# Kernel optimization log

Hardware: AMD Instinct MI355X
Metric: run time of the kernel (lower is better)

## Reference

```python
import jax, jax.numpy as jnp
import numpy as np

N, E, F, R, S = 20000, 320000, 64, 8, 10
AVG_NEIGH = 16.0


def setup_inputs() -> dict:
    key = jax.random.key(0)
    ks = jax.random.split(key, 16)
    inp = {
        "vectors": jax.random.normal(ks[0], (E, 3), jnp.float32),
        "node_feats": jax.random.normal(ks[1], (N, F, 4), jnp.float32),  # [N, F, 1(0e)+3(1o)]
        "node_specie": jax.random.randint(ks[2], (N,), 0, S),
        "radial_embedding": jax.random.normal(ks[3], (E, R), jnp.float32),
        "senders": jax.random.randint(ks[4], (E,), 0, N),
        "receivers": jax.random.randint(ks[5], (E,), 0, N),
        # residual FullyConnectedTensorProduct(feats, one-hot species 0e) == species-dep. linear per l
        "W_res_s": jax.random.normal(ks[6], (S, F, F), jnp.float32),
        "W_res_v": jax.random.normal(ks[7], (S, F, F), jnp.float32),
        # interaction block: input linear per l
        "W_in_s": jax.random.normal(ks[8], (F, F), jnp.float32),
        "W_in_v": jax.random.normal(ks[9], (F, F), jnp.float32),
        # radial MLP -> 5 CG tensor-product path weights per channel
        "mlp_w1": jax.random.normal(ks[10], (R, 64), jnp.float32),
        "mlp_w2": jax.random.normal(ks[11], (64, 5 * F), jnp.float32) / 8.0,
        # interaction block: output linear per l
        "W_out_s": jax.random.normal(ks[12], (F, F), jnp.float32),
        "W_out_v": jax.random.normal(ks[13], (F, F), jnp.float32),
        # symmetric product basis (correlation 3), species-dependent term weights
        "W_prod_s": jax.random.normal(ks[14], (S, 5, F), jnp.float32) * 0.3,
        "W_prod_v": jax.random.normal(ks[15], (S, 4, F), jnp.float32) * 0.3,
    }
    k2 = jax.random.split(jax.random.key(1), 3)
    inp["W_lin_s"] = jax.random.normal(k2[0], (F, F), jnp.float32)
    inp["W_lin_v"] = jax.random.normal(k2[1], (F, F), jnp.float32)
    inp["W_read"] = jax.random.normal(k2[2], (F, 1), jnp.float32)
    return inp


def _forward(vectors, node_feats, node_specie, radial_embedding, senders, receivers,
             W_res_s, W_res_v, W_in_s, W_in_v, mlp_w1, mlp_w2, W_out_s, W_out_v,
             W_prod_s, W_prod_v, W_lin_s, W_lin_v, W_read):
    inv_sf = 1.0 / jnp.sqrt(jnp.float32(F))
    s = node_feats[..., 0]          # [N,F]   0e channels
    v = node_feats[..., 1:]         # [N,F,3] 1o channels

    # --- residual connection: FCTP(feats, one-hot species 0e attrs) -> species-gated linear per l
    res_s = jnp.einsum('nf,ngf->ng', s, W_res_s[node_specie]) * inv_sf
    res_v = jnp.einsum('nfc,ngf->ngc', v, W_res_v[node_specie]) * inv_sf

    # --- InteractionBlock ---
    h_s = (s @ W_in_s) * inv_sf
    h_v = jnp.einsum('nfc,fg->ngc', v, W_in_v) * inv_sf

    # spherical harmonics up to max_ell=1: Y0 = 1, Y1 = unit edge vector
    r = jnp.sqrt(jnp.sum(vectors * vectors, -1) + 1e-12)
    Y1 = vectors / r[:, None]                                # [E,3]

    # radial MLP produces per-edge weights for the 5 CG paths:
    # (0e x Y0 -> 0e), (1o . Y1 -> 0e), (0e x Y1 -> 1o), (1o x Y0 -> 1o), (1o x Y1 -> 1o, cross)
    w = (jax.nn.silu(radial_embedding @ mlp_w1) @ mlp_w2).reshape(-1, 5, F)  # [E,5,F]

    ss = h_s[senders]                                        # [E,F]
    sv = h_v[senders]                                        # [E,F,3]
    dot = jnp.einsum('efc,ec->ef', sv, Y1)                   # [E,F]
    m_s = w[:, 0] * ss + w[:, 1] * dot                       # [E,F]
    m_v = (w[:, 2] * ss)[:, :, None] * Y1[:, None, :] \
        + w[:, 3][:, :, None] * sv \
        + w[:, 4][:, :, None] * jnp.cross(sv, Y1[:, None, :])  # [E,F,3]

    agg_s = jnp.zeros_like(h_s).at[receivers].add(m_s) / AVG_NEIGH
    agg_v = jnp.zeros_like(h_v).at[receivers].add(m_v) / AVG_NEIGH
    a_s = (agg_s @ W_out_s) * inv_sf
    a_v = jnp.einsum('nfc,fg->ngc', agg_v, W_out_v) * inv_sf

    # --- EquivariantProductBasisBlock: correlation-3 symmetric contraction, species-dependent ---
    vv = jnp.sum(a_v * a_v, -1)                              # [N,F] invariant |v|^2
    Wp = W_prod_s[node_specie]                               # [N,5,F]
    p_s = (Wp[:, 0] * a_s + Wp[:, 1] * a_s ** 2 + Wp[:, 2] * a_s ** 3
           + Wp[:, 3] * vv + Wp[:, 4] * a_s * vv)
    Wv = W_prod_v[node_specie]                               # [N,4,F]
    p_v = (Wv[:, 0] + Wv[:, 1] * a_s + Wv[:, 2] * a_s ** 2 + Wv[:, 3] * vv)[:, :, None] * a_v

    f_s = (p_s @ W_lin_s) * inv_sf + res_s
    f_v = jnp.einsum('nfc,fg->ngc', p_v, W_lin_v) * inv_sf + res_v

    # --- LinearReadoutBlock (output_irreps = 0e), 1 head ---
    node_out = ((f_s @ W_read) * inv_sf)[:, None, :]         # [N, heads=1, 1]
    new_feats = jnp.concatenate([f_s[..., None], f_v], axis=-1)  # [N,F,4]
    return node_out, new_feats


def reference(vectors, node_feats, node_specie, radial_embedding, senders, receivers,
              W_res_s, W_res_v, W_in_s, W_in_v, mlp_w1, mlp_w2, W_out_s, W_out_v,
              W_prod_s, W_prod_v, W_lin_s, W_lin_v, W_read):
    return _forward(vectors, node_feats, node_specie, radial_embedding, senders, receivers,
                    W_res_s, W_res_v, W_in_s, W_in_v, mlp_w1, mlp_w2, W_out_s, W_out_v,
                    W_prod_s, W_prod_v, W_lin_s, W_lin_v, W_read)
```

## Files before the change

### kernel.cpp

```cpp
#include <hip/hip_runtime.h>
#include <math.h>

#define NN 20000
#define NE 320000
#define NF (NN*64)
#define TB 16

typedef float v2f __attribute__((ext_vector_type(2)));

#if __has_builtin(__builtin_elementwise_fma)
#define PKFMA(a,b,c) __builtin_elementwise_fma(a,b,c)
#else
static __device__ __forceinline__ v2f PKFMA(v2f a, v2f b, v2f c){
  v2f r; r.x = fmaf(a.x,b.x,c.x); r.y = fmaf(a.y,b.y,c.y); return r;
}
#endif

__global__ __launch_bounds__(256) void k_pre(
    const float* __restrict__ node_feats, const float* __restrict__ W_in_s,
    const float* __restrict__ W_in_v, float* __restrict__ h,
    const int* __restrict__ receivers, int* __restrict__ count, int* __restrict__ rank,
    const float* __restrict__ Ws, const float* __restrict__ Wv,
    float* __restrict__ Wst, float* __restrict__ Wvt)
{
  __shared__ float sh[16][4][64];
  if(blockIdx.x >= 1250){
    int b = blockIdx.x - 1250;
    int e = b*256 + threadIdx.x;
    rank[e] = atomicAdd(&count[receivers[e]], 1);
    if(b < 160){
      int i = b*256 + threadIdx.x;
      int spec = i >> 12;
      int g = (i >> 6) & 63;
      int f = i & 63;
      Wst[spec*4096 + f*64 + g] = Ws[i];
      Wvt[spec*4096 + f*64 + g] = Wv[i];
    }
    return;
  }
  int wave = threadIdx.x >> 6, lane = threadIdx.x & 63;
  int nb = blockIdx.x*16 + wave*4;
  #pragma unroll
  for(int k=0;k<4;++k){
    int nd = wave*4 + k;
    float4 nf = *(const float4*)(node_feats + (size_t)((nb+k)*64 + lane)*4);
    sh[nd][0][lane]=nf.x; sh[nd][1][lane]=nf.y; sh[nd][2][lane]=nf.z; sh[nd][3][lane]=nf.w;
  }
  __syncthreads();
  float as[4]={0,0,0,0}, a0[4]={0,0,0,0}, a1[4]={0,0,0,0}, a2[4]={0,0,0,0};
  for(int f=0; f<64; ++f){
    float ws = W_in_s[f*64+lane], wv = W_in_v[f*64+lane];
    #pragma unroll
    for(int k=0;k<4;++k){
      int nd = wave*4 + k;
      as[k] = fmaf(sh[nd][0][f], ws, as[k]);
      a0[k] = fmaf(sh[nd][1][f], wv, a0[k]);
      a1[k] = fmaf(sh[nd][2][f], wv, a1[k]);
      a2[k] = fmaf(sh[nd][3][f], wv, a2[k]);
    }
  }
  #pragma unroll
  for(int k=0;k<4;++k){
    float4 o4; o4.x = as[k]*0.125f; o4.y = a0[k]*0.125f;
    o4.z = a1[k]*0.125f; o4.w = a2[k]*0.125f;
    *(float4*)(h + (size_t)((nb+k)*64 + lane)*4) = o4;
  }
}

__global__ __launch_bounds__(1024) void k_scan(const int* __restrict__ count,
                                               int* __restrict__ offset)
{
  __shared__ int part[1024];
  int t = threadIdx.x;
  const int PER = 20;
  int base = t*PER;
  int loc[PER];
  int s = 0;
  #pragma unroll
  for(int i=0;i<PER;++i){
    int idx = base+i;
    int v = (idx < NN) ? count[idx] : 0;
    loc[i] = v; s += v;
  }
  part[t] = s;
  __syncthreads();
  for(int off=1; off<1024; off<<=1){
    int v = (t>=off) ? part[t-off] : 0;
    __syncthreads();
    part[t] += v;
    __syncthreads();
  }
  int run = t ? part[t-1] : 0;
  #pragma unroll
  for(int i=0;i<PER;++i){
    int idx = base+i;
    if(idx < NN) offset[idx] = run;
    run += loc[i];
  }
  if(t==1023) offset[NN] = part[1023];
}

__global__ __launch_bounds__(256) void k_scatter(
    const int* __restrict__ senders, const int* __restrict__ receivers,
    const float* __restrict__ vectors, const float* __restrict__ radial,
    const int* __restrict__ offset, const int* __restrict__ rank,
    float* __restrict__ rec)
{
  int e = blockIdx.x*256 + threadIdx.x;
  int r = receivers[e];
  int slot = offset[r] + rank[e];
  float vx = vectors[e*3], vy = vectors[e*3+1], vz = vectors[e*3+2];
  float rinv = rsqrtf(vx*vx + vy*vy + vz*vz + 1e-12f);
  float4 ra = *(const float4*)(radial + (size_t)e*8);
  float4 rb = *(const float4*)(radial + (size_t)e*8 + 4);
  float* rp = rec + (size_t)slot*16;
  float4 w0; w0.x = vx*rinv; w0.y = vy*rinv; w0.z = vz*rinv; w0.w = __int_as_float(senders[e]);
  float4 w3; w3.x = __int_as_float(r); w3.y = 0.f; w3.z = 0.f; w3.w = 0.f;
  *(float4*)(rp)      = w0;
  *(float4*)(rp + 4)  = ra;
  *(float4*)(rp + 8)  = rb;
  *(float4*)(rp + 12) = w3;
}

__global__ __launch_bounds__(256) void k_edge(
    const float* __restrict__ rec,
    const float* __restrict__ mlp_w1, const float* __restrict__ mlp_w2,
    const float* __restrict__ h, float* __restrict__ agg)
{
  __shared__ float recS[4][256];
  __shared__ float hid[4][64][18];
  int tid = threadIdx.x;
  int wave = tid >> 6, lane = tid & 63;
  int e0 = (blockIdx.x*4 + wave)*TB;

  *(float4*)&recS[wave][lane*4] = *(const float4*)(rec + (size_t)e0*16 + lane*4);

  float wl[8];
  #pragma unroll
  for(int r=0;r<8;++r) wl[r] = mlp_w1[r*64+lane];

  #pragma unroll
  for(int t=0;t<TB;++t){
    float acc = 0.f;
    #pragma unroll
    for(int r=0;r<8;++r) acc = fmaf(recS[wave][t*16+4+r], wl[r], acc);
    hid[wave][lane][t] = acc / (1.f + __expf(-acc));
  }

  float as_=0.f, av0=0.f, av1=0.f, av2=0.f;
  int cur = __float_as_int(recS[wave][12]);

  #pragma unroll 1
  for(int half=0; half<2; ++half){
    int tb = half*8;

    float4 hv4[8];
    #pragma unroll
    for(int p=0;p<8;++p){
      int snd = __float_as_int(recS[wave][(tb+p)*16+3]);
      hv4[p] = *(const float4*)(h + (size_t)(snd*64 + lane)*4);
    }

    v2f wv[5][4];
    #pragma unroll
    for(int j=0;j<5;++j)
      #pragma unroll
      for(int tp=0;tp<4;++tp) wv[j][tp] = (v2f){0.f, 0.f};

    for(int hh=0; hh<64; hh+=2){
      float b0[5], b1[5];
      #pragma unroll
      for(int j=0;j<5;++j){
        b0[j] = mlp_w2[hh*320     + j*64 + lane];
        b1[j] = mlp_w2[(hh+1)*320 + j*64 + lane];
      }
      #pragma unroll
      for(int tp=0;tp<4;++tp){
        v2f h0 = *(const v2f*)&hid[wave][hh][tb + 2*tp];
        v2f h1 = *(const v2f*)&hid[wave][hh+1][tb + 2*tp];
        #pragma unroll
        for(int j=0;j<5;++j){
          v2f bb0 = {b0[j], b0[j]};
          v2f bb1 = {b1[j], b1[j]};
          wv[j][tp] = PKFMA(bb0, h0, wv[j][tp]);
          wv[j][tp] = PKFMA(bb1, h1, wv[j][tp]);
        }
      }
    }

    #pragma unroll
    for(int i=0;i<8;++i){
      int t = tb + i;
      float4 hc = hv4[i];
      int rcv = __float_as_int(recS[wave][t*16+12]);
      if(rcv != cur){
        size_t ro = (size_t)cur*256 + lane;
        atomicAdd(&agg[ro],     as_);
        atomicAdd(&agg[ro+64],  av0);
        atomicAdd(&agg[ro+128], av1);
        atomicAdd(&agg[ro+192], av2);
        as_=0.f; av0=0.f; av1=0.f; av2=0.f;
        cur = rcv;
      }
      float y0=recS[wave][t*16], y1=recS[wave][t*16+1], y2=recS[wave][t*16+2];
      float ss=hc.x, sv0=hc.y, sv1=hc.z, sv2=hc.w;
      float dot = sv0*y0 + sv1*y1 + sv2*y2;
      float wt0 = wv[0][i>>1][i&1], wt1 = wv[1][i>>1][i&1];
      float wt2 = wv[2][i>>1][i&1], wt3 = wv[3][i>>1][i&1], wt4 = wv[4][i>>1][i&1];
      as_ += wt0*ss + wt1*dot;
      float w2s = wt2*ss;
      av0 += w2s*y0 + wt3*sv0 + wt4*(sv1*y2 - sv2*y1);
      av1 += w2s*y1 + wt3*sv1 + wt4*(sv2*y0 - sv0*y2);
      av2 += w2s*y2 + wt3*sv2 + wt4*(sv0*y1 - sv1*y0);
    }
  }
  size_t ro = (size_t)cur*256 + lane;
  atomicAdd(&agg[ro],     as_);
  atomicAdd(&agg[ro+64],  av0);
  atomicAdd(&agg[ro+128], av1);
  atomicAdd(&agg[ro+192], av2);
}

__global__ __launch_bounds__(256) void k_node_post(
  const float* __restrict__ node_feats, const int* __restrict__ specie,
  const float* __restrict__ agg,
  const float* __restrict__ Wrst, const float* __restrict__ Wrvt,
  const float* __restrict__ W_out_s, const float* __restrict__ W_out_v,
  const float* __restrict__ W_prod_s, const float* __restrict__ W_prod_v,
  const float* __restrict__ W_lin_s, const float* __restrict__ W_lin_v,
  const float* __restrict__ W_read, float* __restrict__ out_node,
  float* __restrict__ out_feats)
{
  __shared__ float shA[16][4][64];
  __shared__ float shS[16][4][64];
  int wave = threadIdx.x >> 6, lane = threadIdx.x & 63;
  int nb = blockIdx.x*16 + wave*4;
  #pragma unroll
  for(int k=0;k<4;++k){
    int nd = wave*4 + k;
    size_t o = (size_t)(nb+k)*256 + lane;
    shA[nd][0][lane] = agg[o]      * (1.f/16.f);
    shA[nd][1][lane] = agg[o+64]   * (1.f/16.f);
    shA[nd][2][lane] = agg[o+128]  * (1.f/16.f);
    shA[nd][3][lane] = agg[o+192]  * (1.f/16.f);
    float4 nf = *(const float4*)(node_feats + (size_t)((nb+k)*64 + lane)*4);
    shS[nd][0][lane]=nf.x; shS[nd][1][lane]=nf.y; shS[nd][2][lane]=nf.z; shS[nd][3][lane]=nf.w;
  }
  int spec[4];
  #pragma unroll
  for(int k=0;k<4;++k) spec[k] = specie[nb+k];
  __syncthreads();
  float a_s[4]={0,0,0,0}, a0[4]={0,0,0,0}, a1[4]={0,0,0,0}, a2[4]={0,0,0,0};
  float r_s[4]={0,0,0,0}, r0[4]={0,0,0,0}, r1[4]={0,0,0,0}, r2[4]={0,0,0,0};
  for(int f=0; f<64; ++f){
    float wos = W_out_s[f*64+lane], wov = W_out_v[f*64+lane];
    #pragma unroll
    for(int k=0;k<4;++k){
      int nd = wave*4 + k;
      a_s[k] = fmaf(shA[nd][0][f], wos, a_s[k]);
      a0[k]  = fmaf(shA[nd][1][f], wov, a0[k]);
      a1[k]  = fmaf(shA[nd][2][f], wov, a1[k]);
      a2[k]  = fmaf(shA[nd][3][f], wov, a2[k]);
    }
    #pragma unroll
    for(int k=0;k<4;++k){
      int nd = wave*4 + k;
      float wrs = Wrst[spec[k]*4096 + f*64 + lane];
      float wrv = Wrvt[spec[k]*4096 + f*64 + lane];
      r_s[k] = fmaf(shS[nd][0][f], wrs, r_s[k]);
      r0[k]  = fmaf(shS[nd][1][f], wrv, r0[k]);
      r1[k]  = fmaf(shS[nd][2][f], wrv, r1[k]);
      r2[k]  = fmaf(shS[nd][3][f], wrv, r2[k]);
    }
  }
  __syncthreads();
  #pragma unroll
  for(int k=0;k<4;++k){
    int nd = wave*4 + k;
    float A_s = a_s[k]*0.125f, A0 = a0[k]*0.125f, A1 = a1[k]*0.125f, A2 = a2[k]*0.125f;
    float vv = A0*A0 + A1*A1 + A2*A2;
    float as2 = A_s*A_s;
    const float* Wp = W_prod_s + spec[k]*320;
    float p_s = Wp[lane]*A_s + Wp[64+lane]*as2 + Wp[128+lane]*as2*A_s
              + Wp[192+lane]*vv + Wp[256+lane]*A_s*vv;
    const float* Wq = W_prod_v + spec[k]*256;
    float coef = Wq[lane] + Wq[64+lane]*A_s + Wq[128+lane]*as2 + Wq[192+lane]*vv;
    shS[nd][0][lane] = p_s;
    shS[nd][1][lane] = coef*A0;
    shS[nd][2][lane] = coef*A1;
    shS[nd][3][lane] = coef*A2;
  }
  __syncthreads();
  float lfs[4]={0,0,0,0}, lf0[4]={0,0,0,0}, lf1[4]={0,0,0,0}, lf2[4]={0,0,0,0};
  for(int f=0; f<64; ++f){
    float wls = W_lin_s[f*64+lane], wlv = W_lin_v[f*64+lane];
    #pragma unroll
    for(int k=0;k<4;++k){
      int nd = wave*4 + k;
      lfs[k] = fmaf(shS[nd][0][f], wls, lfs[k]);
      lf0[k] = fmaf(shS[nd][1][f], wlv, lf0[k]);
      lf1[k] = fmaf(shS[nd][2][f], wlv, lf1[k]);
      lf2[k] = fmaf(shS[nd][3][f], wlv, lf2[k]);
    }
  }
  float wr = W_read[lane];
  #pragma unroll
  for(int k=0;k<4;++k){
    int n = nb + k;
    float FS = lfs[k]*0.125f + r_s[k]*0.125f;
    float F0 = lf0[k]*0.125f + r0[k]*0.125f;
    float F1 = lf1[k]*0.125f + r1[k]*0.125f;
    float F2 = lf2[k]*0.125f + r2[k]*0.125f;
    float x = FS * wr;
    #pragma unroll
    for(int off=32; off; off>>=1) x += __shfl_down(x, off);
    if(lane==0) out_node[n] = x*0.125f;
    float4 o4; o4.x=FS; o4.y=F0; o4.z=F1; o4.w=F2;
    *(float4*)(out_feats + (size_t)(n*64+lane)*4) = o4;
  }
}

extern "C" void kernel_launch(void* const* d_in, const int* in_sizes, int n_in,
                              void* d_out, int out_size, void* d_ws, size_t ws_size,
                              hipStream_t stream) {
  const float* vectors    = (const float*)d_in[0];
  const float* node_feats = (const float*)d_in[1];
  const int*   node_specie= (const int*)  d_in[2];
  const float* radial     = (const float*)d_in[3];
  const int*   senders    = (const int*)  d_in[4];
  const int*   receivers  = (const int*)  d_in[5];
  const float* W_res_s    = (const float*)d_in[6];
  const float* W_res_v    = (const float*)d_in[7];
  const float* W_in_s     = (const float*)d_in[8];
  const float* W_in_v     = (const float*)d_in[9];
  const float* mlp_w1     = (const float*)d_in[10];
  const float* mlp_w2     = (const float*)d_in[11];
  const float* W_out_s    = (const float*)d_in[12];
  const float* W_out_v    = (const float*)d_in[13];
  const float* W_prod_s   = (const float*)d_in[14];
  const float* W_prod_v   = (const float*)d_in[15];
  const float* W_lin_s    = (const float*)d_in[16];
  const float* W_lin_v    = (const float*)d_in[17];
  const float* W_read     = (const float*)d_in[18];

  float* ws   = (float*)d_ws;
  float* h    = ws;
  float* agg  = ws + 4*(size_t)NF;
  float* Wrst = ws + 8*(size_t)NF;
  float* Wrvt = Wrst + 40960;
  float* rec  = Wrvt + 40960;
  int*   rank   = (int*)(rec + 16*(size_t)NE);
  int*   offset = rank + NE;
  int*   count  = offset + NN + 1;

  hipMemsetAsync(agg,   0, (size_t)4*NF*sizeof(float), stream);
  hipMemsetAsync(count, 0, (size_t)NN*sizeof(int), stream);
  k_pre<<<2500, 256, 0, stream>>>(node_feats, W_in_s, W_in_v, h,
                                  receivers, count, rank,
                                  W_res_s, W_res_v, Wrst, Wrvt);
  k_scan   <<<1,     1024, 0, stream>>>(count, offset);
  k_scatter<<<NE/256, 256, 0, stream>>>(senders, receivers, vectors, radial,
                                        offset, rank, rec);
  k_edge<<<NE/64, 256, 0, stream>>>(rec, mlp_w1, mlp_w2, h, agg);
  k_node_post<<<NN/16, 256, 0, stream>>>(node_feats, node_specie, agg,
                                         Wrst, Wrvt, W_out_s, W_out_v,
                                         W_prod_s, W_prod_v, W_lin_s, W_lin_v,
                                         W_read, (float*)d_out, (float*)d_out + NN);
}
```

Baseline: 465.1 us.

## Compute all 16 edge weights in one pass and double node tiles per block

The edge kernel now computes the radial MLP second layer for all 16 edges in a single loop over the hidden dimension instead of two halves. Each mlp_w2 load is reused across twice as many edges. The sender feature gathers are rotated as a four-deep prefetch ring inside the aggregation loop. The node pre and post kernels process 8 nodes per wave instead of 4, doubling weight reuse per load. The cost is much higher register pressure (80 accumulator floats in the edge kernel, 64 in node_post) and more LDS, which may lower occupancy.

Result: no change. 474.3 us (+2.0%).

```diff
diff --git a/kernel.cpp b/kernel.cpp
--- a/kernel.cpp
+++ b/kernel.cpp
@@ -23,9 +23,9 @@
     const float* __restrict__ Ws, const float* __restrict__ Wv,
     float* __restrict__ Wst, float* __restrict__ Wvt)
 {
-  __shared__ float sh[16][4][64];
-  if(blockIdx.x >= 1250){
-    int b = blockIdx.x - 1250;
+  __shared__ float sh[32][4][64];
+  if(blockIdx.x >= 625){
+    int b = blockIdx.x - 625;
     int e = b*256 + threadIdx.x;
     rank[e] = atomicAdd(&count[receivers[e]], 1);
     if(b < 160){
@@ -39,20 +39,21 @@
     return;
   }
   int wave = threadIdx.x >> 6, lane = threadIdx.x & 63;
-  int nb = blockIdx.x*16 + wave*4;
-  #pragma unroll
-  for(int k=0;k<4;++k){
-    int nd = wave*4 + k;
+  int nb = blockIdx.x*32 + wave*8;
+  #pragma unroll
+  for(int k=0;k<8;++k){
+    int nd = wave*8 + k;
     float4 nf = *(const float4*)(node_feats + (size_t)((nb+k)*64 + lane)*4);
     sh[nd][0][lane]=nf.x; sh[nd][1][lane]=nf.y; sh[nd][2][lane]=nf.z; sh[nd][3][lane]=nf.w;
   }
   __syncthreads();
-  float as[4]={0,0,0,0}, a0[4]={0,0,0,0}, a1[4]={0,0,0,0}, a2[4]={0,0,0,0};
+  float as[8]={0,0,0,0,0,0,0,0}, a0[8]={0,0,0,0,0,0,0,0};
+  float a1[8]={0,0,0,0,0,0,0,0}, a2[8]={0,0,0,0,0,0,0,0};
   for(int f=0; f<64; ++f){
     float ws = W_in_s[f*64+lane], wv = W_in_v[f*64+lane];
     #pragma unroll
-    for(int k=0;k<4;++k){
-      int nd = wave*4 + k;
+    for(int k=0;k<8;++k){
+      int nd = wave*8 + k;
       as[k] = fmaf(sh[nd][0][f], ws, as[k]);
       a0[k] = fmaf(sh[nd][1][f], wv, a0[k]);
       a1[k] = fmaf(sh[nd][2][f], wv, a1[k]);
@@ -60,7 +61,7 @@
     }
   }
   #pragma unroll
-  for(int k=0;k<4;++k){
+  for(int k=0;k<8;++k){
     float4 o4; o4.x = as[k]*0.125f; o4.y = a0[k]*0.125f;
     o4.z = a1[k]*0.125f; o4.w = a2[k]*0.125f;
     *(float4*)(h + (size_t)((nb+k)*64 + lane)*4) = o4;
@@ -128,7 +129,7 @@
     const float* __restrict__ h, float* __restrict__ agg)
 {
   __shared__ float recS[4][256];
-  __shared__ float hid[4][64][18];
+  __shared__ float hid[4][64][20];
   int tid = threadIdx.x;
   int wave = tid >> 6, lane = tid & 63;
   int e0 = (blockIdx.x*4 + wave)*TB;
@@ -147,72 +148,63 @@
     hid[wave][lane][t] = acc / (1.f + __expf(-acc));
   }
 
+  v2f wv[5][8];
+  #pragma unroll
+  for(int j=0;j<5;++j)
+    #pragma unroll
+    for(int tp=0;tp<8;++tp) wv[j][tp] = (v2f){0.f, 0.f};
+  const float* w2p = mlp_w2 + lane;
+  for(int hh=0; hh<64; ++hh){
+    float b[5];
+    #pragma unroll
+    for(int j=0;j<5;++j) b[j] = w2p[hh*320 + j*64];
+    v2f hv[8];
+    #pragma unroll
+    for(int tp=0;tp<8;++tp) hv[tp] = *(const v2f*)&hid[wave][hh][2*tp];
+    #pragma unroll
+    for(int j=0;j<5;++j){
+      v2f bb = {b[j], b[j]};
+      #pragma unroll
+      for(int tp=0;tp<8;++tp) wv[j][tp] = PKFMA(bb, hv[tp], wv[j][tp]);
+    }
+  }
+
+  float4 hv4[4];
+  #pragma unroll
+  for(int p=0;p<4;++p){
+    int snd = __float_as_int(recS[wave][p*16+3]);
+    hv4[p] = *(const float4*)(h + (size_t)(snd*64 + lane)*4);
+  }
+
   float as_=0.f, av0=0.f, av1=0.f, av2=0.f;
   int cur = __float_as_int(recS[wave][12]);
-
-  #pragma unroll 1
-  for(int half=0; half<2; ++half){
-    int tb = half*8;
-
-    float4 hv4[8];
-    #pragma unroll
-    for(int p=0;p<8;++p){
-      int snd = __float_as_int(recS[wave][(tb+p)*16+3]);
-      hv4[p] = *(const float4*)(h + (size_t)(snd*64 + lane)*4);
-    }
-
-    v2f wv[5][4];
-    #pragma unroll
-    for(int j=0;j<5;++j)
-      #pragma unroll
-      for(int tp=0;tp<4;++tp) wv[j][tp] = (v2f){0.f, 0.f};
-
-    for(int hh=0; hh<64; hh+=2){
-      float b0[5], b1[5];
-      #pragma unroll
-      for(int j=0;j<5;++j){
-        b0[j] = mlp_w2[hh*320     + j*64 + lane];
-        b1[j] = mlp_w2[(hh+1)*320 + j*64 + lane];
-      }
-      #pragma unroll
-      for(int tp=0;tp<4;++tp){
-        v2f h0 = *(const v2f*)&hid[wave][hh][tb + 2*tp];
-        v2f h1 = *(const v2f*)&hid[wave][hh+1][tb + 2*tp];
-        #pragma unroll
-        for(int j=0;j<5;++j){
-          v2f bb0 = {b0[j], b0[j]};
-          v2f bb1 = {b1[j], b1[j]};
-          wv[j][tp] = PKFMA(bb0, h0, wv[j][tp]);
-          wv[j][tp] = PKFMA(bb1, h1, wv[j][tp]);
-        }
-      }
-    }
-
-    #pragma unroll
-    for(int i=0;i<8;++i){
-      int t = tb + i;
-      float4 hc = hv4[i];
-      int rcv = __float_as_int(recS[wave][t*16+12]);
-      if(rcv != cur){
-        size_t ro = (size_t)cur*256 + lane;
-        atomicAdd(&agg[ro],     as_);
-        atomicAdd(&agg[ro+64],  av0);
-        atomicAdd(&agg[ro+128], av1);
-        atomicAdd(&agg[ro+192], av2);
-        as_=0.f; av0=0.f; av1=0.f; av2=0.f;
-        cur = rcv;
-      }
-      float y0=recS[wave][t*16], y1=recS[wave][t*16+1], y2=recS[wave][t*16+2];
-      float ss=hc.x, sv0=hc.y, sv1=hc.z, sv2=hc.w;
-      float dot = sv0*y0 + sv1*y1 + sv2*y2;
-      float wt0 = wv[0][i>>1][i&1], wt1 = wv[1][i>>1][i&1];
-      float wt2 = wv[2][i>>1][i&1], wt3 = wv[3][i>>1][i&1], wt4 = wv[4][i>>1][i&1];
-      as_ += wt0*ss + wt1*dot;
-      float w2s = wt2*ss;
-      av0 += w2s*y0 + wt3*sv0 + wt4*(sv1*y2 - sv2*y1);
-      av1 += w2s*y1 + wt3*sv1 + wt4*(sv2*y0 - sv0*y2);
-      av2 += w2s*y2 + wt3*sv2 + wt4*(sv0*y1 - sv1*y0);
-    }
+  #pragma unroll
+  for(int t=0;t<TB;++t){
+    float4 hc = hv4[t&3];
+    if(t+4 < TB){
+      int snd = __float_as_int(recS[wave][(t+4)*16+3]);
+      hv4[t&3] = *(const float4*)(h + (size_t)(snd*64 + lane)*4);
+    }
+    int rcv = __float_as_int(recS[wave][t*16+12]);
+    if(rcv != cur){
+      size_t ro = (size_t)cur*256 + lane;
+      atomicAdd(&agg[ro],     as_);
+      atomicAdd(&agg[ro+64],  av0);
+      atomicAdd(&agg[ro+128], av1);
+      atomicAdd(&agg[ro+192], av2);
+      as_=0.f; av0=0.f; av1=0.f; av2=0.f;
+      cur = rcv;
+    }
+    float y0=recS[wave][t*16], y1=recS[wave][t*16+1], y2=recS[wave][t*16+2];
+    float ss=hc.x, sv0=hc.y, sv1=hc.z, sv2=hc.w;
+    float dot = sv0*y0 + sv1*y1 + sv2*y2;
+    float wt0 = wv[0][t>>1][t&1], wt1 = wv[1][t>>1][t&1];
+    float wt2 = wv[2][t>>1][t&1], wt3 = wv[3][t>>1][t&1], wt4 = wv[4][t>>1][t&1];
+    as_ += wt0*ss + wt1*dot;
+    float w2s = wt2*ss;
+    av0 += w2s*y0 + wt3*sv0 + wt4*(sv1*y2 - sv2*y1);
+    av1 += w2s*y1 + wt3*sv1 + wt4*(sv2*y0 - sv0*y2);
+    av2 += w2s*y2 + wt3*sv2 + wt4*(sv0*y1 - sv1*y0);
   }
   size_t ro = (size_t)cur*256 + lane;
   atomicAdd(&agg[ro],     as_);
@@ -231,13 +223,13 @@
   const float* __restrict__ W_read, float* __restrict__ out_node,
   float* __restrict__ out_feats)
 {
-  __shared__ float shA[16][4][64];
-  __shared__ float shS[16][4][64];
+  __shared__ float shA[32][4][64];
+  __shared__ float shS[32][4][64];
   int wave = threadIdx.x >> 6, lane = threadIdx.x & 63;
-  int nb = blockIdx.x*16 + wave*4;
-  #pragma unroll
-  for(int k=0;k<4;++k){
-    int nd = wave*4 + k;
+  int nb = blockIdx.x*32 + wave*8;
+  #pragma unroll
+  for(int k=0;k<8;++k){
+    int nd = wave*8 + k;
     size_t o = (size_t)(nb+k)*256 + lane;
     shA[nd][0][lane] = agg[o]      * (1.f/16.f);
     shA[nd][1][lane] = agg[o+64]   * (1.f/16.f);
@@ -246,25 +238,27 @@
     float4 nf = *(const float4*)(node_feats + (size_t)((nb+k)*64 + lane)*4);
     shS[nd][0][lane]=nf.x; shS[nd][1][lane]=nf.y; shS[nd][2][lane]=nf.z; shS[nd][3][lane]=nf.w;
   }
-  int spec[4];
-  #pragma unroll
-  for(int k=0;k<4;++k) spec[k] = specie[nb+k];
-  __syncthreads();
-  float a_s[4]={0,0,0,0}, a0[4]={0,0,0,0}, a1[4]={0,0,0,0}, a2[4]={0,0,0,0};
-  float r_s[4]={0,0,0,0}, r0[4]={0,0,0,0}, r1[4]={0,0,0,0}, r2[4]={0,0,0,0};
+  int spec[8];
+  #pragma unroll
+  for(int k=0;k<8;++k) spec[k] = specie[nb+k];
+  __syncthreads();
+  float a_s[8]={0,0,0,0,0,0,0,0}, a0[8]={0,0,0,0,0,0,0,0};
+  float a1[8]={0,0,0,0,0,0,0,0}, a2[8]={0,0,0,0,0,0,0,0};
+  float r_s[8]={0,0,0,0,0,0,0,0}, r0[8]={0,0,0,0,0,0,0,0};
+  float r1[8]={0,0,0,0,0,0,0,0}, r2[8]={0,0,0,0,0,0,0,0};
   for(int f=0; f<64; ++f){
     float wos = W_out_s[f*64+lane], wov = W_out_v[f*64+lane];
     #pragma unroll
-    for(int k=0;k<4;++k){
-      int nd = wave*4 + k;
+    for(int k=0;k<8;++k){
+      int nd = wave*8 + k;
       a_s[k] = fmaf(shA[nd][0][f], wos, a_s[k]);
       a0[k]  = fmaf(shA[nd][1][f], wov, a0[k]);
       a1[k]  = fmaf(shA[nd][2][f], wov, a1[k]);
       a2[k]  = fmaf(shA[nd][3][f], wov, a2[k]);
     }
     #pragma unroll
-    for(int k=0;k<4;++k){
-      int nd = wave*4 + k;
+    for(int k=0;k<8;++k){
+      int nd = wave*8 + k;
       float wrs = Wrst[spec[k]*4096 + f*64 + lane];
       float wrv = Wrvt[spec[k]*4096 + f*64 + lane];
       r_s[k] = fmaf(shS[nd][0][f], wrs, r_s[k]);
@@ -275,8 +269,8 @@
   }
   __syncthreads();
   #pragma unroll
-  for(int k=0;k<4;++k){
-    int nd = wave*4 + k;
+  for(int k=0;k<8;++k){
+    int nd = wave*8 + k;
     float A_s = a_s[k]*0.125f, A0 = a0[k]*0.125f, A1 = a1[k]*0.125f, A2 = a2[k]*0.125f;
     float vv = A0*A0 + A1*A1 + A2*A2;
     float as2 = A_s*A_s;
@@ -291,12 +285,13 @@
     shS[nd][3][lane] = coef*A2;
   }
   __syncthreads();
-  float lfs[4]={0,0,0,0}, lf0[4]={0,0,0,0}, lf1[4]={0,0,0,0}, lf2[4]={0,0,0,0};
+  float lfs[8]={0,0,0,0,0,0,0,0}, lf0[8]={0,0,0,0,0,0,0,0};
+  float lf1[8]={0,0,0,0,0,0,0,0}, lf2[8]={0,0,0,0,0,0,0,0};
   for(int f=0; f<64; ++f){
     float wls = W_lin_s[f*64+lane], wlv = W_lin_v[f*64+lane];
     #pragma unroll
-    for(int k=0;k<4;++k){
-      int nd = wave*4 + k;
+    for(int k=0;k<8;++k){
+      int nd = wave*8 + k;
       lfs[k] = fmaf(shS[nd][0][f], wls, lfs[k]);
       lf0[k] = fmaf(shS[nd][1][f], wlv, lf0[k]);
       lf1[k] = fmaf(shS[nd][2][f], wlv, lf1[k]);
@@ -305,7 +300,7 @@
   }
   float wr = W_read[lane];
   #pragma unroll
-  for(int k=0;k<4;++k){
+  for(int k=0;k<8;++k){
     int n = nb + k;
     float FS = lfs[k]*0.125f + r_s[k]*0.125f;
     float F0 = lf0[k]*0.125f + r0[k]*0.125f;
@@ -355,15 +350,15 @@
 
   hipMemsetAsync(agg,   0, (size_t)4*NF*sizeof(float), stream);
   hipMemsetAsync(count, 0, (size_t)NN*sizeof(int), stream);
-  k_pre<<<2500, 256, 0, stream>>>(node_feats, W_in_s, W_in_v, h,
+  k_pre<<<1875, 256, 0, stream>>>(node_feats, W_in_s, W_in_v, h,
                                   receivers, count, rank,
                                   W_res_s, W_res_v, Wrst, Wrvt);
   k_scan   <<<1,     1024, 0, stream>>>(count, offset);
   k_scatter<<<NE/256, 256, 0, stream>>>(senders, receivers, vectors, radial,
                                         offset, rank, rec);
   k_edge<<<NE/64, 256, 0, stream>>>(rec, mlp_w1, mlp_w2, h, agg);
-  k_node_post<<<NN/16, 256, 0, stream>>>(node_feats, node_specie, agg,
-                                         Wrst, Wrvt, W_out_s, W_out_v,
-                                         W_prod_s, W_prod_v, W_lin_s, W_lin_v,
-                                         W_read, (float*)d_out, (float*)d_out + NN);
-}
+  k_node_post<<<625, 256, 0, stream>>>(node_feats, node_specie, agg,
+                                       Wrst, Wrvt, W_out_s, W_out_v,
+                                       W_prod_s, W_prod_v, W_lin_s, W_lin_v,
+                                       W_read, (float*)d_out, (float*)d_out + NN);
+}
```

## Compute all 16 edge weights in one pass with relaid-out MLP weights

Applied to the files above, without the earlier changes.

The second radial MLP layer now runs over all 16 edges of a wave in a single pass instead of two halves. Each hh step loads its five weights with one vector load from a per-lane padded copy of mlp_w2 that k_pre builds, so mlp_w2 is read once rather than twice. Sender feature gathers use a four-deep rolling prefetch instead of eight loads per half. The single pass doubles the accumulator registers to 80 floats, which may lower occupancy, and the hid row is padded to 20 floats so the float4 reads from shared memory stay aligned.

After: 472.1 us. About the same (+1.5%).

```diff
diff --git a/kernel.cpp b/kernel.cpp
--- a/kernel.cpp
+++ b/kernel.cpp
@@ -21,7 +21,8 @@
     const float* __restrict__ W_in_v, float* __restrict__ h,
     const int* __restrict__ receivers, int* __restrict__ count, int* __restrict__ rank,
     const float* __restrict__ Ws, const float* __restrict__ Wv,
-    float* __restrict__ Wst, float* __restrict__ Wvt)
+    float* __restrict__ Wst, float* __restrict__ Wvt,
+    const float* __restrict__ w2, float* __restrict__ w2r)
 {
   __shared__ float sh[16][4][64];
   if(blockIdx.x >= 1250){
@@ -35,6 +36,13 @@
       int f = i & 63;
       Wst[spec*4096 + f*64 + g] = Ws[i];
       Wvt[spec*4096 + f*64 + g] = Wv[i];
+    } else if(b < 288){
+      int i = (b-160)*256 + threadIdx.x;
+      int hh = i >> 9;
+      int r  = i & 511;
+      int ln = r >> 3;
+      int j  = r & 7;
+      w2r[i] = (j < 5) ? w2[hh*320 + j*64 + ln] : 0.f;
     }
     return;
   }
@@ -124,11 +132,11 @@
 
 __global__ __launch_bounds__(256) void k_edge(
     const float* __restrict__ rec,
-    const float* __restrict__ mlp_w1, const float* __restrict__ mlp_w2,
+    const float* __restrict__ mlp_w1, const float* __restrict__ w2r,
     const float* __restrict__ h, float* __restrict__ agg)
 {
   __shared__ float recS[4][256];
-  __shared__ float hid[4][64][18];
+  __shared__ float hid[4][64][20];
   int tid = threadIdx.x;
   int wave = tid >> 6, lane = tid & 63;
   int e0 = (blockIdx.x*4 + wave)*TB;
@@ -147,72 +155,69 @@
     hid[wave][lane][t] = acc / (1.f + __expf(-acc));
   }
 
+  v2f wv[5][8];
+  #pragma unroll
+  for(int j=0;j<5;++j)
+    #pragma unroll
+    for(int tp=0;tp<8;++tp) wv[j][tp] = (v2f){0.f, 0.f};
+  const float* w2p = w2r + (size_t)lane*8;
+  for(int hh=0; hh<64; ++hh){
+    float4 b04 = *(const float4*)(w2p + hh*512);
+    float  b4  = w2p[hh*512 + 4];
+    float b[5] = {b04.x, b04.y, b04.z, b04.w, b4};
+    float4 q0 = *(const float4*)&hid[wave][hh][0];
+    float4 q1 = *(const float4*)&hid[wave][hh][4];
+    float4 q2 = *(const float4*)&hid[wave][hh][8];
+    float4 q3 = *(const float4*)&hid[wave][hh][12];
+    v2f hv[8];
+    hv[0] = (v2f){q0.x, q0.y}; hv[1] = (v2f){q0.z, q0.w};
+    hv[2] = (v2f){q1.x, q1.y}; hv[3] = (v2f){q1.z, q1.w};
+    hv[4] = (v2f){q2.x, q2.y}; hv[5] = (v2f){q2.z, q2.w};
+    hv[6] = (v2f){q3.x, q3.y}; hv[7] = (v2f){q3.z, q3.w};
+    #pragma unroll
+    for(int j=0;j<5;++j){
+      v2f bb = {b[j], b[j]};
+      #pragma unroll
+      for(int tp=0;tp<8;++tp) wv[j][tp] = PKFMA(bb, hv[tp], wv[j][tp]);
+    }
+  }
+
+  float4 hv4[4];
+  #pragma unroll
+  for(int p=0;p<4;++p){
+    int snd = __float_as_int(recS[wave][p*16+3]);
+    hv4[p] = *(const float4*)(h + (size_t)(snd*64 + lane)*4);
+  }
+
   float as_=0.f, av0=0.f, av1=0.f, av2=0.f;
   int cur = __float_as_int(recS[wave][12]);
-
-  #pragma unroll 1
-  for(int half=0; half<2; ++half){
-    int tb = half*8;
-
-    float4 hv4[8];
-    #pragma unroll
-    for(int p=0;p<8;++p){
-      int snd = __float_as_int(recS[wave][(tb+p)*16+3]);
-      hv4[p] = *(const float4*)(h + (size_t)(snd*64 + lane)*4);
-    }
-
-    v2f wv[5][4];
-    #pragma unroll
-    for(int j=0;j<5;++j)
-      #pragma unroll
-      for(int tp=0;tp<4;++tp) wv[j][tp] = (v2f){0.f, 0.f};
-
-    for(int hh=0; hh<64; hh+=2){
-      float b0[5], b1[5];
-      #pragma unroll
-      for(int j=0;j<5;++j){
-        b0[j] = mlp_w2[hh*320     + j*64 + lane];
-        b1[j] = mlp_w2[(hh+1)*320 + j*64 + lane];
-      }
-      #pragma unroll
-      for(int tp=0;tp<4;++tp){
-        v2f h0 = *(const v2f*)&hid[wave][hh][tb + 2*tp];
-        v2f h1 = *(const v2f*)&hid[wave][hh+1][tb + 2*tp];
-        #pragma unroll
-        for(int j=0;j<5;++j){
-          v2f bb0 = {b0[j], b0[j]};
-          v2f bb1 = {b1[j], b1[j]};
-          wv[j][tp] = PKFMA(bb0, h0, wv[j][tp]);
-          wv[j][tp] = PKFMA(bb1, h1, wv[j][tp]);
-        }
-      }
-    }
-
-    #pragma unroll
-    for(int i=0;i<8;++i){
-      int t = tb + i;
-      float4 hc = hv4[i];
-      int rcv = __float_as_int(recS[wave][t*16+12]);
-      if(rcv != cur){
-        size_t ro = (size_t)cur*256 + lane;
-        atomicAdd(&agg[ro],     as_);
-        atomicAdd(&agg[ro+64],  av0);
-        atomicAdd(&agg[ro+128], av1);
-        atomicAdd(&agg[ro+192], av2);
-        as_=0.f; av0=0.f; av1=0.f; av2=0.f;
-        cur = rcv;
-      }
-      float y0=recS[wave][t*16], y1=recS[wave][t*16+1], y2=recS[wave][t*16+2];
-      float ss=hc.x, sv0=hc.y, sv1=hc.z, sv2=hc.w;
-      float dot = sv0*y0 + sv1*y1 + sv2*y2;
-      float wt0 = wv[0][i>>1][i&1], wt1 = wv[1][i>>1][i&1];
-      float wt2 = wv[2][i>>1][i&1], wt3 = wv[3][i>>1][i&1], wt4 = wv[4][i>>1][i&1];
-      as_ += wt0*ss + wt1*dot;
-      float w2s = wt2*ss;
-      av0 += w2s*y0 + wt3*sv0 + wt4*(sv1*y2 - sv2*y1);
-      av1 += w2s*y1 + wt3*sv1 + wt4*(sv2*y0 - sv0*y2);
-      av2 += w2s*y2 + wt3*sv2 + wt4*(sv0*y1 - sv1*y0);
-    }
+  #pragma unroll
+  for(int t=0;t<TB;++t){
+    float4 hc = hv4[t&3];
+    if(t+4 < TB){
+      int snd = __float_as_int(recS[wave][(t+4)*16+3]);
+      hv4[t&3] = *(const float4*)(h + (size_t)(snd*64 + lane)*4);
+    }
+    int rcv = __float_as_int(recS[wave][t*16+12]);
+    if(rcv != cur){
+      size_t ro = (size_t)cur*256 + lane;
+      atomicAdd(&agg[ro],     as_);
+      atomicAdd(&agg[ro+64],  av0);
+      atomicAdd(&agg[ro+128], av1);
+      atomicAdd(&agg[ro+192], av2);
+      as_=0.f; av0=0.f; av1=0.f; av2=0.f;
+      cur = rcv;
+    }
+    float y0=recS[wave][t*16], y1=recS[wave][t*16+1], y2=recS[wave][t*16+2];
+    float ss=hc.x, sv0=hc.y, sv1=hc.z, sv2=hc.w;
+    float dot = sv0*y0 + sv1*y1 + sv2*y2;
+    float wt0 = wv[0][t>>1][t&1], wt1 = wv[1][t>>1][t&1];
+    float wt2 = wv[2][t>>1][t&1], wt3 = wv[3][t>>1][t&1], wt4 = wv[4][t>>1][t&1];
+    as_ += wt0*ss + wt1*dot;
+    float w2s = wt2*ss;
+    av0 += w2s*y0 + wt3*sv0 + wt4*(sv1*y2 - sv2*y1);
+    av1 += w2s*y1 + wt3*sv1 + wt4*(sv2*y0 - sv0*y2);
+    av2 += w2s*y2 + wt3*sv2 + wt4*(sv0*y1 - sv1*y0);
   }
   size_t ro = (size_t)cur*256 + lane;
   atomicAdd(&agg[ro],     as_);
@@ -349,7 +354,8 @@
   float* Wrst = ws + 8*(size_t)NF;
   float* Wrvt = Wrst + 40960;
   float* rec  = Wrvt + 40960;
-  int*   rank   = (int*)(rec + 16*(size_t)NE);
+  float* w2r  = rec + 16*(size_t)NE;
+  int*   rank   = (int*)(w2r + 32768);
   int*   offset = rank + NE;
   int*   count  = offset + NN + 1;
 
@@ -357,11 +363,12 @@
   hipMemsetAsync(count, 0, (size_t)NN*sizeof(int), stream);
   k_pre<<<2500, 256, 0, stream>>>(node_feats, W_in_s, W_in_v, h,
                                   receivers, count, rank,
-                                  W_res_s, W_res_v, Wrst, Wrvt);
+                                  W_res_s, W_res_v, Wrst, Wrvt,
+                                  mlp_w2, w2r);
   k_scan   <<<1,     1024, 0, stream>>>(count, offset);
   k_scatter<<<NE/256, 256, 0, stream>>>(senders, receivers, vectors, radial,
                                         offset, rank, rec);
-  k_edge<<<NE/64, 256, 0, stream>>>(rec, mlp_w1, mlp_w2, h, agg);
+  k_edge<<<NE/64, 256, 0, stream>>>(rec, mlp_w1, w2r, h, agg);
   k_node_post<<<NN/16, 256, 0, stream>>>(node_feats, node_specie, agg,
                                          Wrst, Wrvt, W_out_s, W_out_v,
                                          W_prod_s, W_prod_v, W_lin_s, W_lin_v,
```
